# Kernel optimization log

Measured on AMD Instinct MI355X. Metric: run time of the kernel, lower is better.

The kernel has to match this reference:

```python
import jax, jax.numpy as jnp
from jax import lax
import numpy as np

B, S, D, H = 64, 1024, 512, 512


def setup_inputs() -> dict:
    key = jax.random.key(0)
    ks = jax.random.split(key, 9)
    scale = 1.0 / np.sqrt(D + H)
    def lin(k):
        kw, kb = jax.random.split(k)
        W = jax.random.uniform(kw, (D + H, H), jnp.float32, -scale, scale)
        b = jax.random.uniform(kb, (H,), jnp.float32, -scale, scale)
        return W, b
    Wf, bf = lin(ks[1])
    Wi, bi = lin(ks[2])
    Wc, bc = lin(ks[3])
    Wo, bo = lin(ks[4])
    x = jax.random.normal(ks[0], (B, S, D), jnp.float32)
    return {"x": x, "Wf": Wf, "bf": bf, "Wi": Wi, "bi": bi,
            "Wc": Wc, "bc": bc, "Wo": Wo, "bo": bo}


def reference(x, Wf, bf, Wi, bi, Wc, bc, Wo, bo):
    batch = x.shape[0]
    hdim = Wf.shape[1]
    h0 = jnp.zeros((batch, hdim), x.dtype)
    c0 = jnp.zeros((batch, hdim), x.dtype)

    def step(carry, xt):
        h, c = carry
        comb = jnp.concatenate([h, xt], axis=-1)  # [B, H+D]
        f = jax.nn.sigmoid(comb @ Wf + bf)
        i = jax.nn.sigmoid(comb @ Wi + bi)
        g = jnp.tanh(comb @ Wc + bc)
        o = jax.nn.sigmoid(comb @ Wo + bo)
        c = c * f + g * i
        h = o * jnp.tanh(c)
        return (h, c), h

    xs = jnp.swapaxes(x, 0, 1)  # [S, B, D]
    (h, c), hs = lax.scan(step, (h0, c0), xs)
    hidden_out = jnp.swapaxes(hs, 0, 1)  # [B, S, H]
    return hidden_out, (h, c)
```

## Files before the change

kernel.cpp:

```cpp
#include <hip/hip_runtime.h>
#include <hip/hip_bf16.h>

#define B_   64
#define S_   1024
#define D_   512
#define H_   512
#define NWG  256
#define NCS  64
#define HCW  8
#define NT   64

typedef __attribute__((ext_vector_type(8))) short short8;
typedef __attribute__((ext_vector_type(4))) float f32x4;

__device__ __forceinline__ int wl_byte(int gc, int k) {
  return ((gc << 11) + (k << 1)) ^ ((gc & 7) << 4);
}
__device__ __forceinline__ float sigm(float v) { return 1.0f / (1.0f + __expf(-v)); }
__device__ __forceinline__ float tanh_(float v) { return 1.0f - 2.0f / (__expf(2.0f * v) + 1.0f); }
__device__ __forceinline__ short f2bf(float f) {
  __hip_bfloat16 h = __float2bfloat16(f);
  short s;
  __builtin_memcpy(&s, &h, 2);
  return s;
}

union U128 { unsigned long long u[2]; unsigned int w[4]; short8 s; };

__device__ __forceinline__ void store_b128_dev(void* p, short8 v) {
  asm volatile("global_store_dwordx4 %0, %1, off sc1" :: "v"(p), "v"(v) : "memory");
}

__global__ __launch_bounds__(256, 1) void lstm_xprep(
    const float* __restrict__ xg, short* __restrict__ xb)
{
  const size_t i = ((size_t)blockIdx.x * 256 + threadIdx.x) * 8;
  f32x4 a = *(const f32x4*)(xg + i);
  f32x4 b = *(const f32x4*)(xg + i + 4);
  short8 v;
#pragma unroll
  for (int j = 0; j < 4; ++j) { v[j] = f2bf(a[j]); v[4 + j] = f2bf(b[j]); }
  *(short8*)(xb + i) = v;
}


template<int USE_XB>
__global__ __launch_bounds__(NT, 1) void lstm_persist(
    const float* __restrict__ xg, const short* __restrict__ xb,
    const float* __restrict__ Wf, const float* __restrict__ bfv,
    const float* __restrict__ Wi, const float* __restrict__ biv,
    const float* __restrict__ Wc, const float* __restrict__ bcv,
    const float* __restrict__ Wo, const float* __restrict__ bov,
    float* __restrict__ out,
    char* __restrict__ hbc)
{
  __shared__ short Wl[32 * 1024];

  const int tid  = threadIdx.x;
  const int wg   = blockIdx.x;
  const int cs   = wg >> 2;
  const int rc   = wg & 3;
  const int lane = tid;

  {
    const float* Wg4[4] = {Wf, Wi, Wc, Wo};
    const int gc  = tid >> 1;
    const int seg = tid & 1;
    const float* Wsrc = Wg4[gc >> 3];
    const int col = cs * HCW + (gc & 7);
    for (int kk = 0; kk < 512; ++kk) {
      const int k = seg * 512 + kk;
      *(short*)((char*)Wl + wl_byte(gc, k)) = f2bf(Wsrc[(size_t)k * H_ + col]);
    }
  }

  const int q    = lane >> 4;
  const int rr   = lane & 15;
  const int c0   = (q & 1) << 2;
  const int colq = cs * HCW + c0;
  float bF4[4], bI4[4], bG4[4], bO4[4];
#pragma unroll
  for (int r = 0; r < 4; ++r) {
    bF4[r] = bfv[colq + r]; bI4[r] = biv[colq + r];
    bG4[r] = bcv[colq + r]; bO4[r] = bov[colq + r];
  }

  __syncthreads();

  const int rowb = (rc << 4) + rr;
  const int kb8  = q << 3;

  float cst[4] = {0.f, 0.f, 0.f, 0.f};

  for (int t = 0; t < S_; ++t) {
    const char* hrd = hbc + (t & 1) * (B_ * NCS * 16);
    char*       hwr = hbc + ((t + 1) & 1) * (B_ * NCS * 16);

    f32x4 acc0 = {0.f, 0.f, 0.f, 0.f};
    f32x4 acc1 = {0.f, 0.f, 0.f, 0.f};

    if constexpr (USE_XB) {
      const short* xr = xb + (size_t)rowb * S_ * D_ + (size_t)t * D_;
#pragma unroll 4
      for (int ks = 0; ks < 16; ++ks) {
        const int kx = ks * 32 + kb8;
        short8 a = *(const short8*)(xr + kx);
        const int kw = 512 + kx;
        short8 b0 = *(const short8*)((const char*)Wl + wl_byte(lane & 15, kw));
        short8 b1 = *(const short8*)((const char*)Wl + wl_byte(16 + (lane & 15), kw));
        acc0 = __builtin_amdgcn_mfma_f32_16x16x32_bf16(b0, a, acc0, 0, 0, 0);
        acc1 = __builtin_amdgcn_mfma_f32_16x16x32_bf16(b1, a, acc1, 0, 0, 0);
      }
    } else {
      const float* xr = xg + (size_t)rowb * S_ * D_ + (size_t)t * D_;
#pragma unroll 4
      for (int ks = 0; ks < 16; ++ks) {
        const int kx = ks * 32 + kb8;
        f32x4 f0 = *(const f32x4*)(xr + kx);
        f32x4 f1 = *(const f32x4*)(xr + kx + 4);
        short8 a;
#pragma unroll
        for (int j = 0; j < 4; ++j) { a[j] = f2bf(f0[j]); a[4 + j] = f2bf(f1[j]); }
        const int kw = 512 + kx;
        short8 b0 = *(const short8*)((const char*)Wl + wl_byte(lane & 15, kw));
        short8 b1 = *(const short8*)((const char*)Wl + wl_byte(16 + (lane & 15), kw));
        acc0 = __builtin_amdgcn_mfma_f32_16x16x32_bf16(b0, a, acc0, 0, 0, 0);
        acc1 = __builtin_amdgcn_mfma_f32_16x16x32_bf16(b1, a, acc1, 0, 0, 0);
      }
    }

    {
      const char* rb = hrd + (rowb << 10) + (q << 4);
      const unsigned int t0 = (unsigned int)t;
      const unsigned int t1 = (unsigned int)t >> 1;
      U128 rc0, rc1, rc2, rc3, rc4, rc5, rc6, rc7,
           rc8, rc9, rc10, rc11, rc12, rc13, rc14, rc15;
      while (true) {
        asm volatile(
          "global_load_dwordx4 %[r0], %[p], off sc1\n\t"
          "global_load_dwordx4 %[r1], %[p], off offset:64 sc1\n\t"
          "global_load_dwordx4 %[r2], %[p], off offset:128 sc1\n\t"
          "global_load_dwordx4 %[r3], %[p], off offset:192 sc1\n\t"
          "global_load_dwordx4 %[r4], %[p], off offset:256 sc1\n\t"
          "global_load_dwordx4 %[r5], %[p], off offset:320 sc1\n\t"
          "global_load_dwordx4 %[r6], %[p], off offset:384 sc1\n\t"
          "global_load_dwordx4 %[r7], %[p], off offset:448 sc1\n\t"
          "global_load_dwordx4 %[r8], %[p], off offset:512 sc1\n\t"
          "global_load_dwordx4 %[r9], %[p], off offset:576 sc1\n\t"
          "global_load_dwordx4 %[r10], %[p], off offset:640 sc1\n\t"
          "global_load_dwordx4 %[r11], %[p], off offset:704 sc1\n\t"
          "global_load_dwordx4 %[r12], %[p], off offset:768 sc1\n\t"
          "global_load_dwordx4 %[r13], %[p], off offset:832 sc1\n\t"
          "global_load_dwordx4 %[r14], %[p], off offset:896 sc1\n\t"
          "global_load_dwordx4 %[r15], %[p], off offset:960 sc1\n\t"
          "s_waitcnt vmcnt(0)"
          : [r0]"=&v"(rc0.s), [r1]"=&v"(rc1.s), [r2]"=&v"(rc2.s),
            [r3]"=&v"(rc3.s), [r4]"=&v"(rc4.s), [r5]"=&v"(rc5.s),
            [r6]"=&v"(rc6.s), [r7]"=&v"(rc7.s), [r8]"=&v"(rc8.s),
            [r9]"=&v"(rc9.s), [r10]"=&v"(rc10.s), [r11]"=&v"(rc11.s),
            [r12]"=&v"(rc12.s), [r13]"=&v"(rc13.s), [r14]"=&v"(rc14.s),
            [r15]"=&v"(rc15.s)
          : [p]"v"(rb)
          : "memory");
#define TCHK(R) ( ((R.w[0] ^ t0) & 1u) | ((R.w[2] ^ t1) & 1u) )
        const unsigned int bad =
            TCHK(rc0)  | TCHK(rc1)  | TCHK(rc2)  | TCHK(rc3)  |
            TCHK(rc4)  | TCHK(rc5)  | TCHK(rc6)  | TCHK(rc7)  |
            TCHK(rc8)  | TCHK(rc9)  | TCHK(rc10) | TCHK(rc11) |
            TCHK(rc12) | TCHK(rc13) | TCHK(rc14) | TCHK(rc15);
#undef TCHK
        if (__all((int)(bad == 0u))) break;
      }

      f32x4 acc0b = {0.f, 0.f, 0.f, 0.f};
      f32x4 acc1b = {0.f, 0.f, 0.f, 0.f};
#define HSTEP(KS, RA, A0, A1)                                                  \
      {                                                                        \
        const int k0_ = (KS) * 32 + kb8;                                       \
        short8 b0_ = *(const short8*)((const char*)Wl + wl_byte(lane & 15, k0_)); \
        short8 b1_ = *(const short8*)((const char*)Wl + wl_byte(16 + (lane & 15), k0_)); \
        A0 = __builtin_amdgcn_mfma_f32_16x16x32_bf16(b0_, RA.s, A0, 0, 0, 0);  \
        A1 = __builtin_amdgcn_mfma_f32_16x16x32_bf16(b1_, RA.s, A1, 0, 0, 0);  \
      }
      HSTEP(0,  rc0,  acc0,  acc1)  HSTEP(1,  rc1,  acc0b, acc1b)
      HSTEP(2,  rc2,  acc0,  acc1)  HSTEP(3,  rc3,  acc0b, acc1b)
      HSTEP(4,  rc4,  acc0,  acc1)  HSTEP(5,  rc5,  acc0b, acc1b)
      HSTEP(6,  rc6,  acc0,  acc1)  HSTEP(7,  rc7,  acc0b, acc1b)
      HSTEP(8,  rc8,  acc0,  acc1)  HSTEP(9,  rc9,  acc0b, acc1b)
      HSTEP(10, rc10, acc0,  acc1)  HSTEP(11, rc11, acc0b, acc1b)
      HSTEP(12, rc12, acc0,  acc1)  HSTEP(13, rc13, acc0b, acc1b)
      HSTEP(14, rc14, acc0,  acc1)  HSTEP(15, rc15, acc0b, acc1b)
#undef HSTEP
#pragma unroll
      for (int j = 0; j < 4; ++j) { acc0[j] += acc0b[j]; acc1[j] += acc1b[j]; }
    }

    f32x4 x0, x1;
#pragma unroll
    for (int j = 0; j < 4; ++j) {
      x0[j] = __shfl_xor(acc0[j], 32);
      x1[j] = __shfl_xor(acc1[j], 32);
    }
    const bool lo = (q < 2);
    float hv[4];
#pragma unroll
    for (int r = 0; r < 4; ++r) {
      const float sF = (lo ? acc0[r] : x0[r]) + bF4[r];
      const float sI = (lo ? x0[r] : acc0[r]) + bI4[r];
      const float sG = (lo ? acc1[r] : x1[r]) + bG4[r];
      const float sO = (lo ? x1[r] : acc1[r]) + bO4[r];
      const float fg = sigm(sF);
      const float ig = sigm(sI);
      const float gg = tanh_(sG);
      const float og = sigm(sO);
      const float cn = cst[r] * fg + gg * ig;
      cst[r] = cn;
      hv[r] = og * tanh_(cn);
    }

    unsigned long long hp8;
    {
      unsigned int l32 = (unsigned int)(unsigned short)f2bf(hv[0])
                       | ((unsigned int)(unsigned short)f2bf(hv[1]) << 16);
      unsigned int h32 = (unsigned int)(unsigned short)f2bf(hv[2])
                       | ((unsigned int)(unsigned short)f2bf(hv[3]) << 16);
      hp8 = (unsigned long long)l32 | ((unsigned long long)h32 << 32);
    }
    unsigned long long other = __shfl_xor(hp8, 16);
    if (q == 0 && t < S_ - 1) {
      const unsigned int tag = (unsigned int)(t + 1);
      U128 u;
      u.w[0] = ((unsigned int)hp8 & ~1u) | (tag & 1u);
      u.w[1] = (unsigned int)(hp8 >> 32);
      u.w[2] = ((unsigned int)other & ~1u) | ((tag >> 1) & 1u);
      u.w[3] = (unsigned int)(other >> 32);
      store_b128_dev(hwr + (rowb << 10) + (cs << 4), u.s);
    }

    if (lo) {
      f32x4 hv4;
#pragma unroll
      for (int r = 0; r < 4; ++r) hv4[r] = hv[r];
      *(f32x4*)(out + (size_t)rowb * ((size_t)S_ * H_) + (size_t)t * H_ + colq) = hv4;
      if (t == S_ - 1) {
        f32x4 c4;
#pragma unroll
        for (int r = 0; r < 4; ++r) c4[r] = cst[r];
        *(f32x4*)(out + (size_t)B_ * S_ * H_ + (size_t)rowb * H_ + colq) = hv4;
        *(f32x4*)(out + (size_t)B_ * S_ * H_ + (size_t)B_ * H_
                      + (size_t)rowb * H_ + colq) = c4;
      }
    }
  }
}

extern "C" void kernel_launch(void* const* d_in, const int* in_sizes, int n_in,
                              void* d_out, int out_size, void* d_ws, size_t ws_size,
                              hipStream_t stream) {
  (void)in_sizes; (void)n_in; (void)out_size;
  const float* x  = (const float*)d_in[0];
  const float* Wf = (const float*)d_in[1];
  const float* bf = (const float*)d_in[2];
  const float* Wi = (const float*)d_in[3];
  const float* bi = (const float*)d_in[4];
  const float* Wc = (const float*)d_in[5];
  const float* bc = (const float*)d_in[6];
  const float* Wo = (const float*)d_in[7];
  const float* bo = (const float*)d_in[8];
  float* out = (float*)d_out;

  char* hbc = (char*)d_ws;

  const size_t XB_OFF   = (size_t)1 << 20;
  const size_t XB_BYTES = (size_t)B_ * S_ * D_ * sizeof(short);

  hipMemsetAsync(d_ws, 0, 2 * B_ * NCS * 16, stream);

  if (ws_size >= XB_OFF + XB_BYTES) {
    short* xb = (short*)((char*)d_ws + XB_OFF);
    lstm_xprep<<<dim3((B_ * S_ * D_) / (256 * 8)), dim3(256), 0, stream>>>(x, xb);
    lstm_persist<1><<<dim3(NWG), dim3(NT), 0, stream>>>(
        x, xb, Wf, bf, Wi, bi, Wc, bc, Wo, bo, out, hbc);
  } else {
    lstm_persist<0><<<dim3(NWG), dim3(NT), 0, stream>>>(
        x, nullptr, Wf, bf, Wi, bi, Wc, bc, Wo, bo, out, hbc);
  }
}
```

Before: 4.201 ms.

## Widen column slices, split batch into cohorts, use XCD-local coherence when possible

Each workgroup now owns 16 hidden columns across all four gates and computes every gate itself, so the cross-half shuffle exchange goes away. Batch rows are split into four independent 16-row cohorts, each with its own h exchange buffer. Only half the launched blocks stay active, which spreads work across XCDs. Blocks record their XCC ID in a claims array, and when a whole cohort sits on one XCD the h exchange uses sc0 loads and stores instead of system-level sc1. This aims to cut polling latency and sync scope per timestep, at the cost of a larger LDS weight footprint and a placement-dependent fast path.

```diff
diff --git a/kernel.cpp b/kernel.cpp
--- a/kernel.cpp
+++ b/kernel.cpp
@@ -6,8 +6,8 @@
 #define D_   512
 #define H_   512
 #define NWG  256
-#define NCS  64
-#define HCW  8
+#define NCS  32
+#define HCW  16
 #define NT   64
 
 typedef __attribute__((ext_vector_type(8))) short short8;
@@ -26,10 +26,6 @@
 }
 
 union U128 { unsigned long long u[2]; unsigned int w[4]; short8 s; };
-
-__device__ __forceinline__ void store_b128_dev(void* p, short8 v) {
-  asm volatile("global_store_dwordx4 %0, %1, off sc1" :: "v"(p), "v"(v) : "memory");
-}
 
 __global__ __launch_bounds__(256, 1) void lstm_xprep(
     const float* __restrict__ xg, short* __restrict__ xb)
@@ -52,32 +48,29 @@
     const float* __restrict__ Wc, const float* __restrict__ bcv,
     const float* __restrict__ Wo, const float* __restrict__ bov,
     float* __restrict__ out,
-    char* __restrict__ hbc)
+    char* __restrict__ hbc,
+    unsigned int* __restrict__ claims)
 {
-  __shared__ short Wl[32 * 1024];
-
-  const int tid  = threadIdx.x;
-  const int wg   = blockIdx.x;
-  const int cs   = wg >> 2;
-  const int rc   = wg & 3;
-  const int lane = tid;
+  __shared__ short Wl[64 * 1024];
+
+  const int bid    = blockIdx.x;
+  const int cohort = bid & 7;
+  if (cohort >= 4) return;
+  const int cs   = bid >> 3;
+  const int lane = threadIdx.x;
 
   {
     const float* Wg4[4] = {Wf, Wi, Wc, Wo};
-    const int gc  = tid >> 1;
-    const int seg = tid & 1;
-    const float* Wsrc = Wg4[gc >> 3];
-    const int col = cs * HCW + (gc & 7);
-    for (int kk = 0; kk < 512; ++kk) {
-      const int k = seg * 512 + kk;
+    const int gc = lane;
+    const float* Wsrc = Wg4[gc >> 4];
+    const int col = cs * HCW + (gc & 15);
+    for (int k = 0; k < 1024; ++k)
       *(short*)((char*)Wl + wl_byte(gc, k)) = f2bf(Wsrc[(size_t)k * H_ + col]);
-    }
   }
 
   const int q    = lane >> 4;
   const int rr   = lane & 15;
-  const int c0   = (q & 1) << 2;
-  const int colq = cs * HCW + c0;
+  const int colq = cs * HCW + (q << 2);
   float bF4[4], bI4[4], bG4[4], bO4[4];
 #pragma unroll
   for (int r = 0; r < 4; ++r) {
@@ -85,19 +78,34 @@
     bG4[r] = bcv[colq + r]; bO4[r] = bov[colq + r];
   }
 
+  const int rowb = (cohort << 4) + rr;
+  const int kb8  = q << 3;
+
+  int xcd;
+  asm volatile("s_getreg_b32 %0, hwreg(HW_REG_XCC_ID)" : "=s"(xcd));
+  if (lane == 0)
+    __hip_atomic_store(&claims[(cohort << 5) + cs], (unsigned int)(xcd + 1),
+                       __ATOMIC_RELAXED, __HIP_MEMORY_SCOPE_SYSTEM);
+  unsigned int mine;
+  do {
+    mine = __hip_atomic_load(&claims[(cohort << 5) + (lane & 31)],
+                             __ATOMIC_RELAXED, __HIP_MEMORY_SCOPE_SYSTEM);
+  } while (!__all((int)(mine != 0u)));
+  const unsigned int ref = (unsigned int)__shfl((int)mine, 0);
+  const bool use_sc0 = (__all((int)(mine == ref)) != 0);
+
   __syncthreads();
 
-  const int rowb = (rc << 4) + rr;
-  const int kb8  = q << 3;
+  char* cb = hbc + (cohort << 14);
 
   float cst[4] = {0.f, 0.f, 0.f, 0.f};
 
   for (int t = 0; t < S_; ++t) {
-    const char* hrd = hbc + (t & 1) * (B_ * NCS * 16);
-    char*       hwr = hbc + ((t + 1) & 1) * (B_ * NCS * 16);
-
-    f32x4 acc0 = {0.f, 0.f, 0.f, 0.f};
-    f32x4 acc1 = {0.f, 0.f, 0.f, 0.f};
+    const char* hrd = cb + (t & 1) * 65536;
+    char*       hwr = cb + ((t + 1) & 1) * 65536;
+
+    f32x4 aF = {0.f,0.f,0.f,0.f}, aI = {0.f,0.f,0.f,0.f};
+    f32x4 aG = {0.f,0.f,0.f,0.f}, aO = {0.f,0.f,0.f,0.f};
 
     if constexpr (USE_XB) {
       const short* xr = xb + (size_t)rowb * S_ * D_ + (size_t)t * D_;
@@ -106,10 +114,14 @@
         const int kx = ks * 32 + kb8;
         short8 a = *(const short8*)(xr + kx);
         const int kw = 512 + kx;
-        short8 b0 = *(const short8*)((const char*)Wl + wl_byte(lane & 15, kw));
-        short8 b1 = *(const short8*)((const char*)Wl + wl_byte(16 + (lane & 15), kw));
-        acc0 = __builtin_amdgcn_mfma_f32_16x16x32_bf16(b0, a, acc0, 0, 0, 0);
-        acc1 = __builtin_amdgcn_mfma_f32_16x16x32_bf16(b1, a, acc1, 0, 0, 0);
+        short8 bF = *(const short8*)((const char*)Wl + wl_byte(rr, kw));
+        short8 bI = *(const short8*)((const char*)Wl + wl_byte(16 + rr, kw));
+        short8 bG = *(const short8*)((const char*)Wl + wl_byte(32 + rr, kw));
+        short8 bO = *(const short8*)((const char*)Wl + wl_byte(48 + rr, kw));
+        aF = __builtin_amdgcn_mfma_f32_16x16x32_bf16(bF, a, aF, 0, 0, 0);
+        aI = __builtin_amdgcn_mfma_f32_16x16x32_bf16(bI, a, aI, 0, 0, 0);
+        aG = __builtin_amdgcn_mfma_f32_16x16x32_bf16(bG, a, aG, 0, 0, 0);
+        aO = __builtin_amdgcn_mfma_f32_16x16x32_bf16(bO, a, aO, 0, 0, 0);
       }
     } else {
       const float* xr = xg + (size_t)rowb * S_ * D_ + (size_t)t * D_;
@@ -122,97 +134,89 @@
 #pragma unroll
         for (int j = 0; j < 4; ++j) { a[j] = f2bf(f0[j]); a[4 + j] = f2bf(f1[j]); }
         const int kw = 512 + kx;
-        short8 b0 = *(const short8*)((const char*)Wl + wl_byte(lane & 15, kw));
-        short8 b1 = *(const short8*)((const char*)Wl + wl_byte(16 + (lane & 15), kw));
-        acc0 = __builtin_amdgcn_mfma_f32_16x16x32_bf16(b0, a, acc0, 0, 0, 0);
-        acc1 = __builtin_amdgcn_mfma_f32_16x16x32_bf16(b1, a, acc1, 0, 0, 0);
-      }
-    }
-
+        short8 bF = *(const short8*)((const char*)Wl + wl_byte(rr, kw));
+        short8 bI = *(const short8*)((const char*)Wl + wl_byte(16 + rr, kw));
+        short8 bG = *(const short8*)((const char*)Wl + wl_byte(32 + rr, kw));
+        short8 bO = *(const short8*)((const char*)Wl + wl_byte(48 + rr, kw));
+        aF = __builtin_amdgcn_mfma_f32_16x16x32_bf16(bF, a, aF, 0, 0, 0);
+        aI = __builtin_amdgcn_mfma_f32_16x16x32_bf16(bI, a, aI, 0, 0, 0);
+        aG = __builtin_amdgcn_mfma_f32_16x16x32_bf16(bG, a, aG, 0, 0, 0);
+        aO = __builtin_amdgcn_mfma_f32_16x16x32_bf16(bO, a, aO, 0, 0, 0);
+      }
+    }
+
+    U128 rc0, rc1, rc2, rc3, rc4, rc5, rc6, rc7,
+         rc8, rc9, rc10, rc11, rc12, rc13, rc14, rc15;
     {
-      const char* rb = hrd + (rowb << 10) + (q << 4);
+      const char* rb = hrd + (rr << 10) + (q << 4);
       const unsigned int t0 = (unsigned int)t;
       const unsigned int t1 = (unsigned int)t >> 1;
-      U128 rc0, rc1, rc2, rc3, rc4, rc5, rc6, rc7,
-           rc8, rc9, rc10, rc11, rc12, rc13, rc14, rc15;
-      while (true) {
-        asm volatile(
-          "global_load_dwordx4 %[r0], %[p], off sc1\n\t"
-          "global_load_dwordx4 %[r1], %[p], off offset:64 sc1\n\t"
-          "global_load_dwordx4 %[r2], %[p], off offset:128 sc1\n\t"
-          "global_load_dwordx4 %[r3], %[p], off offset:192 sc1\n\t"
-          "global_load_dwordx4 %[r4], %[p], off offset:256 sc1\n\t"
-          "global_load_dwordx4 %[r5], %[p], off offset:320 sc1\n\t"
-          "global_load_dwordx4 %[r6], %[p], off offset:384 sc1\n\t"
-          "global_load_dwordx4 %[r7], %[p], off offset:448 sc1\n\t"
-          "global_load_dwordx4 %[r8], %[p], off offset:512 sc1\n\t"
-          "global_load_dwordx4 %[r9], %[p], off offset:576 sc1\n\t"
-          "global_load_dwordx4 %[r10], %[p], off offset:640 sc1\n\t"
-          "global_load_dwordx4 %[r11], %[p], off offset:704 sc1\n\t"
-          "global_load_dwordx4 %[r12], %[p], off offset:768 sc1\n\t"
-          "global_load_dwordx4 %[r13], %[p], off offset:832 sc1\n\t"
-          "global_load_dwordx4 %[r14], %[p], off offset:896 sc1\n\t"
-          "global_load_dwordx4 %[r15], %[p], off offset:960 sc1\n\t"
-          "s_waitcnt vmcnt(0)"
-          : [r0]"=&v"(rc0.s), [r1]"=&v"(rc1.s), [r2]"=&v"(rc2.s),
-            [r3]"=&v"(rc3.s), [r4]"=&v"(rc4.s), [r5]"=&v"(rc5.s),
-            [r6]"=&v"(rc6.s), [r7]"=&v"(rc7.s), [r8]"=&v"(rc8.s),
-            [r9]"=&v"(rc9.s), [r10]"=&v"(rc10.s), [r11]"=&v"(rc11.s),
-            [r12]"=&v"(rc12.s), [r13]"=&v"(rc13.s), [r14]"=&v"(rc14.s),
-            [r15]"=&v"(rc15.s)
-          : [p]"v"(rb)
-          : "memory");
 #define TCHK(R) ( ((R.w[0] ^ t0) & 1u) | ((R.w[2] ^ t1) & 1u) )
-        const unsigned int bad =
-            TCHK(rc0)  | TCHK(rc1)  | TCHK(rc2)  | TCHK(rc3)  |
-            TCHK(rc4)  | TCHK(rc5)  | TCHK(rc6)  | TCHK(rc7)  |
-            TCHK(rc8)  | TCHK(rc9)  | TCHK(rc10) | TCHK(rc11) |
-            TCHK(rc12) | TCHK(rc13) | TCHK(rc14) | TCHK(rc15);
+#define POLLBODY(FLAGS)                                                        \
+      while (true) {                                                           \
+        asm volatile(                                                          \
+          "global_load_dwordx4 %[r0], %[p], off " FLAGS "\n\t"                 \
+          "global_load_dwordx4 %[r1], %[p], off offset:64 " FLAGS "\n\t"       \
+          "global_load_dwordx4 %[r2], %[p], off offset:128 " FLAGS "\n\t"      \
+          "global_load_dwordx4 %[r3], %[p], off offset:192 " FLAGS "\n\t"      \
+          "global_load_dwordx4 %[r4], %[p], off offset:256 " FLAGS "\n\t"      \
+          "global_load_dwordx4 %[r5], %[p], off offset:320 " FLAGS "\n\t"      \
+          "global_load_dwordx4 %[r6], %[p], off offset:384 " FLAGS "\n\t"      \
+          "global_load_dwordx4 %[r7], %[p], off offset:448 " FLAGS "\n\t"      \
+          "global_load_dwordx4 %[r8], %[p], off offset:512 " FLAGS "\n\t"      \
+          "global_load_dwordx4 %[r9], %[p], off offset:576 " FLAGS "\n\t"      \
+          "global_load_dwordx4 %[r10], %[p], off offset:640 " FLAGS "\n\t"     \
+          "global_load_dwordx4 %[r11], %[p], off offset:704 " FLAGS "\n\t"     \
+          "global_load_dwordx4 %[r12], %[p], off offset:768 " FLAGS "\n\t"     \
+          "global_load_dwordx4 %[r13], %[p], off offset:832 " FLAGS "\n\t"     \
+          "global_load_dwordx4 %[r14], %[p], off offset:896 " FLAGS "\n\t"     \
+          "global_load_dwordx4 %[r15], %[p], off offset:960 " FLAGS "\n\t"     \
+          "s_waitcnt vmcnt(0)"                                                 \
+          : [r0]"=&v"(rc0.s), [r1]"=&v"(rc1.s), [r2]"=&v"(rc2.s),              \
+            [r3]"=&v"(rc3.s), [r4]"=&v"(rc4.s), [r5]"=&v"(rc5.s),              \
+            [r6]"=&v"(rc6.s), [r7]"=&v"(rc7.s), [r8]"=&v"(rc8.s),              \
+            [r9]"=&v"(rc9.s), [r10]"=&v"(rc10.s), [r11]"=&v"(rc11.s),          \
+            [r12]"=&v"(rc12.s), [r13]"=&v"(rc13.s), [r14]"=&v"(rc14.s),        \
+            [r15]"=&v"(rc15.s)                                                 \
+          : [p]"v"(rb)                                                         \
+          : "memory");                                                         \
+        const unsigned int bad =                                               \
+            TCHK(rc0)  | TCHK(rc1)  | TCHK(rc2)  | TCHK(rc3)  |                \
+            TCHK(rc4)  | TCHK(rc5)  | TCHK(rc6)  | TCHK(rc7)  |                \
+            TCHK(rc8)  | TCHK(rc9)  | TCHK(rc10) | TCHK(rc11) |                \
+            TCHK(rc12) | TCHK(rc13) | TCHK(rc14) | TCHK(rc15);                 \
+        if (__all((int)(bad == 0u))) break;                                    \
+      }
+      if (use_sc0) { POLLBODY("sc0") } else { POLLBODY("sc1") }
+#undef POLLBODY
 #undef TCHK
-        if (__all((int)(bad == 0u))) break;
-      }
-
-      f32x4 acc0b = {0.f, 0.f, 0.f, 0.f};
-      f32x4 acc1b = {0.f, 0.f, 0.f, 0.f};
-#define HSTEP(KS, RA, A0, A1)                                                  \
-      {                                                                        \
-        const int k0_ = (KS) * 32 + kb8;                                       \
-        short8 b0_ = *(const short8*)((const char*)Wl + wl_byte(lane & 15, k0_)); \
-        short8 b1_ = *(const short8*)((const char*)Wl + wl_byte(16 + (lane & 15), k0_)); \
-        A0 = __builtin_amdgcn_mfma_f32_16x16x32_bf16(b0_, RA.s, A0, 0, 0, 0);  \
-        A1 = __builtin_amdgcn_mfma_f32_16x16x32_bf16(b1_, RA.s, A1, 0, 0, 0);  \
-      }
-      HSTEP(0,  rc0,  acc0,  acc1)  HSTEP(1,  rc1,  acc0b, acc1b)
-      HSTEP(2,  rc2,  acc0,  acc1)  HSTEP(3,  rc3,  acc0b, acc1b)
-      HSTEP(4,  rc4,  acc0,  acc1)  HSTEP(5,  rc5,  acc0b, acc1b)
-      HSTEP(6,  rc6,  acc0,  acc1)  HSTEP(7,  rc7,  acc0b, acc1b)
-      HSTEP(8,  rc8,  acc0,  acc1)  HSTEP(9,  rc9,  acc0b, acc1b)
-      HSTEP(10, rc10, acc0,  acc1)  HSTEP(11, rc11, acc0b, acc1b)
-      HSTEP(12, rc12, acc0,  acc1)  HSTEP(13, rc13, acc0b, acc1b)
-      HSTEP(14, rc14, acc0,  acc1)  HSTEP(15, rc15, acc0b, acc1b)
-#undef HSTEP
-#pragma unroll
-      for (int j = 0; j < 4; ++j) { acc0[j] += acc0b[j]; acc1[j] += acc1b[j]; }
-    }
-
-    f32x4 x0, x1;
-#pragma unroll
-    for (int j = 0; j < 4; ++j) {
-      x0[j] = __shfl_xor(acc0[j], 32);
-      x1[j] = __shfl_xor(acc1[j], 32);
-    }
-    const bool lo = (q < 2);
+    }
+
+#define HS(KS, RA)                                                             \
+    {                                                                          \
+      const int k0_ = (KS) * 32 + kb8;                                         \
+      short8 bF_ = *(const short8*)((const char*)Wl + wl_byte(rr, k0_));       \
+      short8 bI_ = *(const short8*)((const char*)Wl + wl_byte(16 + rr, k0_));  \
+      short8 bG_ = *(const short8*)((const char*)Wl + wl_byte(32 + rr, k0_));  \
+      short8 bO_ = *(const short8*)((const char*)Wl + wl_byte(48 + rr, k0_));  \
+      aF = __builtin_amdgcn_mfma_f32_16x16x32_bf16(bF_, RA.s, aF, 0, 0, 0);    \
+      aI = __builtin_amdgcn_mfma_f32_16x16x32_bf16(bI_, RA.s, aI, 0, 0, 0);    \
+      aG = __builtin_amdgcn_mfma_f32_16x16x32_bf16(bG_, RA.s, aG, 0, 0, 0);    \
+      aO = __builtin_amdgcn_mfma_f32_16x16x32_bf16(bO_, RA.s, aO, 0, 0, 0);    \
+    }
+    HS(0,  rc0)  HS(1,  rc1)  HS(2,  rc2)  HS(3,  rc3)
+    HS(4,  rc4)  HS(5,  rc5)  HS(6,  rc6)  HS(7,  rc7)
+    HS(8,  rc8)  HS(9,  rc9)  HS(10, rc10) HS(11, rc11)
+    HS(12, rc12) HS(13, rc13) HS(14, rc14) HS(15, rc15)
+#undef HS
+
     float hv[4];
 #pragma unroll
     for (int r = 0; r < 4; ++r) {
-      const float sF = (lo ? acc0[r] : x0[r]) + bF4[r];
-      const float sI = (lo ? x0[r] : acc0[r]) + bI4[r];
-      const float sG = (lo ? acc1[r] : x1[r]) + bG4[r];
-      const float sO = (lo ? x1[r] : acc1[r]) + bO4[r];
-      const float fg = sigm(sF);
-      const float ig = sigm(sI);
-      const float gg = tanh_(sG);
-      const float og = sigm(sO);
+      const float fg = sigm(aF[r] + bF4[r]);
+      const float ig = sigm(aI[r] + bI4[r]);
+      const float gg = tanh_(aG[r] + bG4[r]);
+      const float og = sigm(aO[r] + bO4[r]);
       const float cn = cst[r] * fg + gg * ig;
       cst[r] = cn;
       hv[r] = og * tanh_(cn);
@@ -226,18 +230,26 @@
                        | ((unsigned int)(unsigned short)f2bf(hv[3]) << 16);
       hp8 = (unsigned long long)l32 | ((unsigned long long)h32 << 32);
     }
-    unsigned long long other = __shfl_xor(hp8, 16);
-    if (q == 0 && t < S_ - 1) {
+    unsigned long long part = __shfl_xor(hp8, 16);
+    if ((q & 1) == 0 && t < S_ - 1) {
+      const int g = (cs << 1) + (q >> 1);
       const unsigned int tag = (unsigned int)(t + 1);
       U128 u;
       u.w[0] = ((unsigned int)hp8 & ~1u) | (tag & 1u);
       u.w[1] = (unsigned int)(hp8 >> 32);
-      u.w[2] = ((unsigned int)other & ~1u) | ((tag >> 1) & 1u);
-      u.w[3] = (unsigned int)(other >> 32);
-      store_b128_dev(hwr + (rowb << 10) + (cs << 4), u.s);
-    }
-
-    if (lo) {
+      u.w[2] = ((unsigned int)part & ~1u) | ((tag >> 1) & 1u);
+      u.w[3] = (unsigned int)(part >> 32);
+      void* dst = hwr + (rr << 10) + (g << 4);
+      if (use_sc0) {
+        asm volatile("global_store_dwordx4 %0, %1, off sc0"
+                     :: "v"(dst), "v"(u.s) : "memory");
+      } else {
+        asm volatile("global_store_dwordx4 %0, %1, off sc1"
+                     :: "v"(dst), "v"(u.s) : "memory");
+      }
+    }
+
+    {
       f32x4 hv4;
 #pragma unroll
       for (int r = 0; r < 4; ++r) hv4[r] = hv[r];
@@ -269,20 +281,21 @@
   const float* bo = (const float*)d_in[8];
   float* out = (float*)d_out;
 
-  char* hbc = (char*)d_ws;
+  unsigned int* claims = (unsigned int*)d_ws;
+  char* hbc = (char*)d_ws + 4096;
 
   const size_t XB_OFF   = (size_t)1 << 20;
   const size_t XB_BYTES = (size_t)B_ * S_ * D_ * sizeof(short);
 
-  hipMemsetAsync(d_ws, 0, 2 * B_ * NCS * 16, stream);
+  hipMemsetAsync(d_ws, 0, 4096 + 2 * 4 * 16384, stream);
 
   if (ws_size >= XB_OFF + XB_BYTES) {
     short* xb = (short*)((char*)d_ws + XB_OFF);
     lstm_xprep<<<dim3((B_ * S_ * D_) / (256 * 8)), dim3(256), 0, stream>>>(x, xb);
     lstm_persist<1><<<dim3(NWG), dim3(NT), 0, stream>>>(
-        x, xb, Wf, bf, Wi, bi, Wc, bc, Wo, bo, out, hbc);
+        x, xb, Wf, bf, Wi, bi, Wc, bc, Wo, bo, out, hbc, claims);
   } else {
     lstm_persist<0><<<dim3(NWG), dim3(NT), 0, stream>>>(
-        x, nullptr, Wf, bf, Wi, bi, Wc, bc, Wo, bo, out, hbc);
+        x, nullptr, Wf, bf, Wi, bi, Wc, bc, Wo, bo, out, hbc, claims);
   }
 }
```

Result: slower. 4.553 ms (+8.4%).

## Prefetch next-step x tile into LDS asynchronously and poll h first

Applied to the files above, without the earlier changes.

In the bf16-x path, the persistent LSTM kernel now uses global_load_lds to prefetch the next timestep's x slice into a double-buffered LDS tile, so the x-projection MFMAs read LDS instead of issuing global loads each step. The spin-poll for the previous step's h records moves ahead of the x-projection, and its vmcnt(0) wait also covers the outstanding prefetch. This takes global x-load latency off each step. In exchange, the x-projection MFMAs now run after the h dependency has resolved instead of overlapping the wait, and the kernel uses more LDS.

```diff
diff --git a/kernel.cpp b/kernel.cpp
--- a/kernel.cpp
+++ b/kernel.cpp
@@ -29,6 +29,12 @@
 
 __device__ __forceinline__ void store_b128_dev(void* p, short8 v) {
   asm volatile("global_store_dwordx4 %0, %1, off sc1" :: "v"(p), "v"(v) : "memory");
+}
+
+__device__ __forceinline__ void gload_lds16(const short* g, short* l) {
+  __builtin_amdgcn_global_load_lds(
+      (const __attribute__((address_space(1))) unsigned int*)(const void*)g,
+      (__attribute__((address_space(3))) unsigned int*)l, 16, 0, 0);
 }
 
 __global__ __launch_bounds__(256, 1) void lstm_xprep(
@@ -55,6 +61,7 @@
     char* __restrict__ hbc)
 {
   __shared__ short Wl[32 * 1024];
+  __shared__ short Xl[2][8192];
 
   const int tid  = threadIdx.x;
   const int wg   = blockIdx.x;
@@ -85,10 +92,17 @@
     bG4[r] = bcv[colq + r]; bO4[r] = bov[colq + r];
   }
 
-  __syncthreads();
-
   const int rowb = (rc << 4) + rr;
   const int kb8  = q << 3;
+
+  if constexpr (USE_XB) {
+    const short* xr0 = xb + (size_t)rowb * S_ * D_;
+#pragma unroll
+    for (int ks = 0; ks < 16; ++ks)
+      gload_lds16(xr0 + ks * 32 + kb8, &Xl[0][ks * 512]);
+  }
+
+  __syncthreads();
 
   float cst[4] = {0.f, 0.f, 0.f, 0.f};
 
@@ -98,14 +112,66 @@
 
     f32x4 acc0 = {0.f, 0.f, 0.f, 0.f};
     f32x4 acc1 = {0.f, 0.f, 0.f, 0.f};
+    U128 rc0, rc1, rc2, rc3, rc4, rc5, rc6, rc7,
+         rc8, rc9, rc10, rc11, rc12, rc13, rc14, rc15;
+
+#define POLL_RECORDS()                                                         \
+    {                                                                          \
+      const char* rb = hrd + (rowb << 10) + (q << 4);                          \
+      const unsigned int t0 = (unsigned int)t;                                 \
+      const unsigned int t1 = (unsigned int)t >> 1;                            \
+      while (true) {                                                           \
+        asm volatile(                                                          \
+          "global_load_dwordx4 %[r0], %[p], off sc1\n\t"                       \
+          "global_load_dwordx4 %[r1], %[p], off offset:64 sc1\n\t"             \
+          "global_load_dwordx4 %[r2], %[p], off offset:128 sc1\n\t"            \
+          "global_load_dwordx4 %[r3], %[p], off offset:192 sc1\n\t"            \
+          "global_load_dwordx4 %[r4], %[p], off offset:256 sc1\n\t"            \
+          "global_load_dwordx4 %[r5], %[p], off offset:320 sc1\n\t"            \
+          "global_load_dwordx4 %[r6], %[p], off offset:384 sc1\n\t"            \
+          "global_load_dwordx4 %[r7], %[p], off offset:448 sc1\n\t"            \
+          "global_load_dwordx4 %[r8], %[p], off offset:512 sc1\n\t"            \
+          "global_load_dwordx4 %[r9], %[p], off offset:576 sc1\n\t"            \
+          "global_load_dwordx4 %[r10], %[p], off offset:640 sc1\n\t"           \
+          "global_load_dwordx4 %[r11], %[p], off offset:704 sc1\n\t"           \
+          "global_load_dwordx4 %[r12], %[p], off offset:768 sc1\n\t"           \
+          "global_load_dwordx4 %[r13], %[p], off offset:832 sc1\n\t"           \
+          "global_load_dwordx4 %[r14], %[p], off offset:896 sc1\n\t"           \
+          "global_load_dwordx4 %[r15], %[p], off offset:960 sc1\n\t"           \
+          "s_waitcnt vmcnt(0)"                                                 \
+          : [r0]"=&v"(rc0.s), [r1]"=&v"(rc1.s), [r2]"=&v"(rc2.s),              \
+            [r3]"=&v"(rc3.s), [r4]"=&v"(rc4.s), [r5]"=&v"(rc5.s),              \
+            [r6]"=&v"(rc6.s), [r7]"=&v"(rc7.s), [r8]"=&v"(rc8.s),              \
+            [r9]"=&v"(rc9.s), [r10]"=&v"(rc10.s), [r11]"=&v"(rc11.s),          \
+            [r12]"=&v"(rc12.s), [r13]"=&v"(rc13.s), [r14]"=&v"(rc14.s),        \
+            [r15]"=&v"(rc15.s)                                                 \
+          : [p]"v"(rb)                                                         \
+          : "memory");                                                         \
+        const unsigned int bad =                                               \
+            TCHK(rc0)  | TCHK(rc1)  | TCHK(rc2)  | TCHK(rc3)  |                \
+            TCHK(rc4)  | TCHK(rc5)  | TCHK(rc6)  | TCHK(rc7)  |                \
+            TCHK(rc8)  | TCHK(rc9)  | TCHK(rc10) | TCHK(rc11) |                \
+            TCHK(rc12) | TCHK(rc13) | TCHK(rc14) | TCHK(rc15);                 \
+        if (__all((int)(bad == 0u))) break;                                    \
+      }                                                                        \
+    }
+#define TCHK(R) ( ((R.w[0] ^ t0) & 1u) | ((R.w[2] ^ t1) & 1u) )
 
     if constexpr (USE_XB) {
-      const short* xr = xb + (size_t)rowb * S_ * D_ + (size_t)t * D_;
+      POLL_RECORDS();
+
+      if (t < S_ - 1) {
+        const short* xr1 = xb + (size_t)rowb * S_ * D_ + (size_t)(t + 1) * D_;
+#pragma unroll
+        for (int ks = 0; ks < 16; ++ks)
+          gload_lds16(xr1 + ks * 32 + kb8, &Xl[(t + 1) & 1][ks * 512]);
+      }
+
+      const short* xl = &Xl[t & 1][lane << 3];
 #pragma unroll 4
       for (int ks = 0; ks < 16; ++ks) {
-        const int kx = ks * 32 + kb8;
-        short8 a = *(const short8*)(xr + kx);
-        const int kw = 512 + kx;
+        short8 a = *(const short8*)(xl + ks * 512);
+        const int kw = 512 + ks * 32 + kb8;
         short8 b0 = *(const short8*)((const char*)Wl + wl_byte(lane & 15, kw));
         short8 b1 = *(const short8*)((const char*)Wl + wl_byte(16 + (lane & 15), kw));
         acc0 = __builtin_amdgcn_mfma_f32_16x16x32_bf16(b0, a, acc0, 0, 0, 0);
@@ -127,51 +193,12 @@
         acc0 = __builtin_amdgcn_mfma_f32_16x16x32_bf16(b0, a, acc0, 0, 0, 0);
         acc1 = __builtin_amdgcn_mfma_f32_16x16x32_bf16(b1, a, acc1, 0, 0, 0);
       }
-    }
+      POLL_RECORDS();
+    }
+#undef TCHK
+#undef POLL_RECORDS
 
     {
-      const char* rb = hrd + (rowb << 10) + (q << 4);
-      const unsigned int t0 = (unsigned int)t;
-      const unsigned int t1 = (unsigned int)t >> 1;
-      U128 rc0, rc1, rc2, rc3, rc4, rc5, rc6, rc7,
-           rc8, rc9, rc10, rc11, rc12, rc13, rc14, rc15;
-      while (true) {
-        asm volatile(
-          "global_load_dwordx4 %[r0], %[p], off sc1\n\t"
-          "global_load_dwordx4 %[r1], %[p], off offset:64 sc1\n\t"
-          "global_load_dwordx4 %[r2], %[p], off offset:128 sc1\n\t"
-          "global_load_dwordx4 %[r3], %[p], off offset:192 sc1\n\t"
-          "global_load_dwordx4 %[r4], %[p], off offset:256 sc1\n\t"
-          "global_load_dwordx4 %[r5], %[p], off offset:320 sc1\n\t"
-          "global_load_dwordx4 %[r6], %[p], off offset:384 sc1\n\t"
-          "global_load_dwordx4 %[r7], %[p], off offset:448 sc1\n\t"
-          "global_load_dwordx4 %[r8], %[p], off offset:512 sc1\n\t"
-          "global_load_dwordx4 %[r9], %[p], off offset:576 sc1\n\t"
-          "global_load_dwordx4 %[r10], %[p], off offset:640 sc1\n\t"
-          "global_load_dwordx4 %[r11], %[p], off offset:704 sc1\n\t"
-          "global_load_dwordx4 %[r12], %[p], off offset:768 sc1\n\t"
-          "global_load_dwordx4 %[r13], %[p], off offset:832 sc1\n\t"
-          "global_load_dwordx4 %[r14], %[p], off offset:896 sc1\n\t"
-          "global_load_dwordx4 %[r15], %[p], off offset:960 sc1\n\t"
-          "s_waitcnt vmcnt(0)"
-          : [r0]"=&v"(rc0.s), [r1]"=&v"(rc1.s), [r2]"=&v"(rc2.s),
-            [r3]"=&v"(rc3.s), [r4]"=&v"(rc4.s), [r5]"=&v"(rc5.s),
-            [r6]"=&v"(rc6.s), [r7]"=&v"(rc7.s), [r8]"=&v"(rc8.s),
-            [r9]"=&v"(rc9.s), [r10]"=&v"(rc10.s), [r11]"=&v"(rc11.s),
-            [r12]"=&v"(rc12.s), [r13]"=&v"(rc13.s), [r14]"=&v"(rc14.s),
-            [r15]"=&v"(rc15.s)
-          : [p]"v"(rb)
-          : "memory");
-#define TCHK(R) ( ((R.w[0] ^ t0) & 1u) | ((R.w[2] ^ t1) & 1u) )
-        const unsigned int bad =
-            TCHK(rc0)  | TCHK(rc1)  | TCHK(rc2)  | TCHK(rc3)  |
-            TCHK(rc4)  | TCHK(rc5)  | TCHK(rc6)  | TCHK(rc7)  |
-            TCHK(rc8)  | TCHK(rc9)  | TCHK(rc10) | TCHK(rc11) |
-            TCHK(rc12) | TCHK(rc13) | TCHK(rc14) | TCHK(rc15);
-#undef TCHK
-        if (__all((int)(bad == 0u))) break;
-      }
-
       f32x4 acc0b = {0.f, 0.f, 0.f, 0.f};
       f32x4 acc1b = {0.f, 0.f, 0.f, 0.f};
 #define HSTEP(KS, RA, A0, A1)                                                  \
```

Result: slower. 5.919 ms (+40.9%).
